# Kernel optimization log

Measured on AMD Instinct MI355X. Metric: run time of the kernel, lower is better.

## Reference

```python
import jax, jax.numpy as jnp
import numpy as np

TAU = 2.0  # aggregator_temp


def setup_inputs() -> dict:
    key = jax.random.key(0)
    k1, k2 = jax.random.split(key)
    B, Na, Nv, D = 32, 512, 256, 384
    audio_feats = jax.random.normal(k1, (B, Na, D), dtype=jnp.float32)
    visual_feats = jax.random.normal(k2, (B, Nv, D), dtype=jnp.float32)
    return {"audio_feats": audio_feats, "visual_feats": visual_feats}


def reference(audio_feats, visual_feats):
    # Cross-batch token similarities: (B, B, Na, Nv)
    # token_sims[i, j, n, m] = <audio_feats[i, n], visual_feats[j, m]>
    token_sims = jnp.einsum('ind,jmd->ijnm', audio_feats, visual_feats)
    # logsumexp_pool: tau * logsumexp(sims / tau) over key-token dim (Nv),
    # then mean over query-token dim (Na) -> clip_sims (B, B)
    aggregator = TAU * jax.nn.logsumexp(token_sims / TAU, axis=-1)
    clip_sims = aggregator.mean(axis=-1)
    return clip_sims
```

## Files before the change

kernel.cpp:

```cpp
#include <hip/hip_runtime.h>

constexpr int B_  = 32;
constexpr int Na  = 512;
constexpr int Nv  = 256;
constexpr int D   = 384;

constexpr int NK2 = D / 64;

constexpr int AGROUPS = B_ * 16;
constexpr int BGROUPS = B_ * 8;
constexpr size_t GROUP_BYTES = 12 * 1024;
constexpr int SCALE_ONE = 0x7F7F7F7F;

typedef int   int4v    __attribute__((ext_vector_type(4)));
typedef int   int8v    __attribute__((ext_vector_type(8)));
typedef float floatx16 __attribute__((ext_vector_type(16)));

__global__ void convert_fp8_kernel(const float* __restrict__ a, const float* __restrict__ v,
                                   unsigned char* __restrict__ a8,
                                   unsigned char* __restrict__ b8,
                                   float* __restrict__ out) {
    int gid = blockIdx.x * blockDim.x + threadIdx.x;
    if (gid < B_ * B_) out[gid] = 0.0f;

    const float* src;
    unsigned char* dst;
    int blk = blockIdx.x;
    if (blk < AGROUPS) {
        src = a + (size_t)blk * 32 * D;
        dst = a8 + (size_t)blk * GROUP_BYTES;
    } else {
        int b2 = blk - AGROUPS;
        src = v + (size_t)b2 * 32 * D;
        dst = b8 + (size_t)b2 * GROUP_BYTES;
    }
    const int t = threadIdx.x;
    const int r = t >> 3, q = t & 7;

    #pragma unroll
    for (int p = 0; p < 3; ++p) {
        int k0 = p * 128 + q * 16;
        const float4* s4 = (const float4*)(src + (size_t)r * D + k0);
        float4 f0 = s4[0], f1 = s4[1], f2 = s4[2], f3 = s4[3];
        int w0 = 0, w1 = 0, w2 = 0, w3 = 0;
        w0 = __builtin_amdgcn_cvt_pk_fp8_f32(f0.x, f0.y, w0, false);
        w0 = __builtin_amdgcn_cvt_pk_fp8_f32(f0.z, f0.w, w0, true);
        w1 = __builtin_amdgcn_cvt_pk_fp8_f32(f1.x, f1.y, w1, false);
        w1 = __builtin_amdgcn_cvt_pk_fp8_f32(f1.z, f1.w, w1, true);
        w2 = __builtin_amdgcn_cvt_pk_fp8_f32(f2.x, f2.y, w2, false);
        w2 = __builtin_amdgcn_cvt_pk_fp8_f32(f2.z, f2.w, w2, true);
        w3 = __builtin_amdgcn_cvt_pk_fp8_f32(f3.x, f3.y, w3, false);
        w3 = __builtin_amdgcn_cvt_pk_fp8_f32(f3.z, f3.w, w3, true);
        int kc = k0 >> 5;
        int h2 = (k0 >> 4) & 1;
        int4v o = { w0, w1, w2, w3 };
        *(int4v*)(dst + (size_t)kc * 1024 + h2 * 512 + r * 16) = o;
    }
}

__device__ __forceinline__ float expsum16(floatx16 a) {
    constexpr float INV_TAU_LN2 = 0.7213475204444817f;
    float e[16];
    #pragma unroll
    for (int i = 0; i < 16; ++i)
        e[i] = __builtin_amdgcn_exp2f(a[i] * INV_TAU_LN2);
    float t0 = (e[0] + e[1])  + (e[2] + e[3]);
    float t1 = (e[4] + e[5])  + (e[6] + e[7]);
    float t2 = (e[8] + e[9])  + (e[10] + e[11]);
    float t3 = (e[12] + e[13]) + (e[14] + e[15]);
    return (t0 + t1) + (t2 + t3);
}

__device__ __forceinline__ int8v mk8(int4v lo, int4v hi) {
    int8v r;
    r[0] = lo[0]; r[1] = lo[1]; r[2] = lo[2]; r[3] = lo[3];
    r[4] = hi[0]; r[5] = hi[1]; r[6] = hi[2]; r[7] = hi[3];
    return r;
}

__global__ __launch_bounds__(256, 3) void gemm_lse_kernel(
        const unsigned char* __restrict__ a8,
        const unsigned char* __restrict__ b8,
        float* __restrict__ out)
{
    __shared__ float ms[4][2][32];

    const int tid  = threadIdx.x;
    const int lane = tid & 63;
    const int vq   = tid >> 6;

    int b = blockIdx.x;
    const int xcd   = b & 7;      b >>= 3;
    const int bi_lo = b & 3;      b >>= 2;
    const int ro    = b & 7;      b >>= 3;
    const int bj    = b;
    const int bi    = xcd * 4 + bi_lo;

    const size_t laneoff = (size_t)lane * 16;
    const unsigned char* pa0 = a8 + (size_t)(bi * 16 + ro * 2) * GROUP_BYTES + laneoff;
    const unsigned char* pa1 = pa0 + GROUP_BYTES;
    const unsigned char* pv0 = b8 + (size_t)(bj * 8 + vq * 2) * GROUP_BYTES + laneoff;
    const unsigned char* pv1 = pv0 + GROUP_BYTES;

    int8v Ab[2][2], Vb[2][2];
    Ab[0][0] = mk8(*(const int4v*)pa0, *(const int4v*)(pa0 + 1024));
    Ab[0][1] = mk8(*(const int4v*)pa1, *(const int4v*)(pa1 + 1024));
    Vb[0][0] = mk8(*(const int4v*)pv0, *(const int4v*)(pv0 + 1024));
    Vb[0][1] = mk8(*(const int4v*)pv1, *(const int4v*)(pv1 + 1024));

    floatx16 acc[2][2];
    #pragma unroll
    for (int ag = 0; ag < 2; ++ag)
        #pragma unroll
        for (int vg = 0; vg < 2; ++vg)
            acc[ag][vg] = (floatx16)(0.0f);

    #pragma unroll
    for (int k = 0; k < NK2; ++k) {
        const int cur = k & 1, nxt = cur ^ 1;
        if (k + 1 < NK2) {
            const size_t o = (size_t)(k + 1) * 2048;
            Ab[nxt][0] = mk8(*(const int4v*)(pa0 + o), *(const int4v*)(pa0 + o + 1024));
            Ab[nxt][1] = mk8(*(const int4v*)(pa1 + o), *(const int4v*)(pa1 + o + 1024));
            Vb[nxt][0] = mk8(*(const int4v*)(pv0 + o), *(const int4v*)(pv0 + o + 1024));
            Vb[nxt][1] = mk8(*(const int4v*)(pv1 + o), *(const int4v*)(pv1 + o + 1024));
        }
        __builtin_amdgcn_sched_barrier(0);
        __builtin_amdgcn_s_setprio(1);
        #pragma unroll
        for (int vg = 0; vg < 2; ++vg) {
            acc[0][vg] = __builtin_amdgcn_mfma_scale_f32_32x32x64_f8f6f4(
                Vb[cur][vg], Ab[cur][0], acc[0][vg], 0, 0, 0, SCALE_ONE, 0, SCALE_ONE);
            acc[1][vg] = __builtin_amdgcn_mfma_scale_f32_32x32x64_f8f6f4(
                Vb[cur][vg], Ab[cur][1], acc[1][vg], 0, 0, 0, SCALE_ONE, 0, SCALE_ONE);
        }
        __builtin_amdgcn_s_setprio(0);
        __builtin_amdgcn_sched_barrier(0);
    }

    float s0 = expsum16(acc[0][0]) + expsum16(acc[0][1]);
    float s1 = expsum16(acc[1][0]) + expsum16(acc[1][1]);
    s0 += __shfl_xor(s0, 32);
    s1 += __shfl_xor(s1, 32);
    if (lane < 32) {
        ms[vq][0][lane] = s0;
        ms[vq][1][lane] = s1;
    }
    __syncthreads();

    if (tid < 64) {
        const int g = tid >> 5, r = tid & 31;
        float e = (ms[0][g][r] + ms[1][g][r]) + (ms[2][g][r] + ms[3][g][r]);
        constexpr float TAU_LN2 = 1.3862943611198906f;
        float lse = TAU_LN2 * __builtin_amdgcn_logf(e);
        #pragma unroll
        for (int m = 1; m < 64; m <<= 1) lse += __shfl_xor(lse, m);
        if (tid == 0)
            atomicAdd(&out[bi * 32 + bj], lse * (1.0f / Na));
    }
}

extern "C" void kernel_launch(void* const* d_in, const int* in_sizes, int n_in,
                              void* d_out, int out_size, void* d_ws, size_t ws_size,
                              hipStream_t stream) {
    const float* audio  = (const float*)d_in[0];
    const float* visual = (const float*)d_in[1];
    float* out = (float*)d_out;

    unsigned char* a8 = (unsigned char*)d_ws;
    unsigned char* b8 = a8 + (size_t)AGROUPS * GROUP_BYTES;

    convert_fp8_kernel<<<dim3(AGROUPS + BGROUPS), dim3(256), 0, stream>>>(
        audio, visual, a8, b8, out);
    gemm_lse_kernel<<<dim3(8192), dim3(256), 0, stream>>>(a8, b8, out);
}
```

Measured before the change: 131.7 us.

## Stage audio tile in LDS via async loads and enlarge blocks to 512 threads

Doubles the block to 8 waves covering 128 audio rows by 256 visual rows. The audio fp8 tile is loaded once per block into 48KB of LDS with global_load_lds, so more waves share it. The visual fp8 layout is changed so each lane reads a contiguous 32-byte int8v per k-step. The explicit register double-buffering and sched barriers are removed, which lowers global traffic for A but adds LDS pressure, an upfront sync, and possibly less overlap of loads with MFMA.

```diff
diff --git a/kernel.cpp b/kernel.cpp
--- a/kernel.cpp
+++ b/kernel.cpp
@@ -16,6 +16,13 @@
 typedef int   int8v    __attribute__((ext_vector_type(8)));
 typedef float floatx16 __attribute__((ext_vector_type(16)));
 
+__device__ __forceinline__ void async_load16(const void* g, void* l) {
+    __builtin_amdgcn_global_load_lds(
+        (const __attribute__((address_space(1))) unsigned int*)g,
+        (__attribute__((address_space(3))) unsigned int*)l,
+        16, 0, 0);
+}
+
 __global__ void convert_fp8_kernel(const float* __restrict__ a, const float* __restrict__ v,
                                    unsigned char* __restrict__ a8,
                                    unsigned char* __restrict__ b8,
@@ -26,7 +33,8 @@
     const float* src;
     unsigned char* dst;
     int blk = blockIdx.x;
-    if (blk < AGROUPS) {
+    const bool isA = blk < AGROUPS;
+    if (isA) {
         src = a + (size_t)blk * 32 * D;
         dst = a8 + (size_t)blk * GROUP_BYTES;
     } else {
@@ -53,8 +61,15 @@
         w3 = __builtin_amdgcn_cvt_pk_fp8_f32(f3.z, f3.w, w3, true);
         int kc = k0 >> 5;
         int h2 = (k0 >> 4) & 1;
+        size_t off;
+        if (isA) {
+            off = (size_t)kc * 1024 + h2 * 512 + r * 16;
+        } else {
+            int q2 = kc >> 1, u = kc & 1, l = r + 32 * h2;
+            off = (size_t)q2 * 2048 + l * 32 + u * 16;
+        }
         int4v o = { w0, w1, w2, w3 };
-        *(int4v*)(dst + (size_t)kc * 1024 + h2 * 512 + r * 16) = o;
+        *(int4v*)(dst + off) = o;
     }
 }
 
@@ -71,42 +86,41 @@
     return (t0 + t1) + (t2 + t3);
 }
 
-__device__ __forceinline__ int8v mk8(int4v lo, int4v hi) {
-    int8v r;
-    r[0] = lo[0]; r[1] = lo[1]; r[2] = lo[2]; r[3] = lo[3];
-    r[4] = hi[0]; r[5] = hi[1]; r[6] = hi[2]; r[7] = hi[3];
-    return r;
-}
-
-__global__ __launch_bounds__(256, 3) void gemm_lse_kernel(
+__global__ __launch_bounds__(512, 4) void gemm_lse_kernel(
         const unsigned char* __restrict__ a8,
         const unsigned char* __restrict__ b8,
         float* __restrict__ out)
 {
-    __shared__ float ms[4][2][32];
+    __shared__ unsigned char ldsA[48 * 1024];
+    __shared__ float ms[4][4][32];
 
     const int tid  = threadIdx.x;
     const int lane = tid & 63;
-    const int vq   = tid >> 6;
+    const int wv   = tid >> 6;
+    const int wm   = wv >> 2;
+    const int wn   = wv & 3;
 
     int b = blockIdx.x;
     const int xcd   = b & 7;      b >>= 3;
     const int bi_lo = b & 3;      b >>= 2;
-    const int ro    = b & 7;      b >>= 3;
+    const int rb    = b & 3;      b >>= 2;
     const int bj    = b;
     const int bi    = xcd * 4 + bi_lo;
 
-    const size_t laneoff = (size_t)lane * 16;
-    const unsigned char* pa0 = a8 + (size_t)(bi * 16 + ro * 2) * GROUP_BYTES + laneoff;
-    const unsigned char* pa1 = pa0 + GROUP_BYTES;
-    const unsigned char* pv0 = b8 + (size_t)(bj * 8 + vq * 2) * GROUP_BYTES + laneoff;
+    const unsigned char* asrc = a8 + (size_t)(bi * 16 + rb * 4) * GROUP_BYTES
+                                   + (size_t)lane * 16;
+    #pragma unroll
+    for (int i = 0; i < 6; ++i) {
+        const int u = wv * 6 + i;
+        async_load16(asrc + (size_t)u * 1024, ldsA + u * 1024);
+    }
+    __syncthreads();
+
+    const unsigned char* pv0 = b8 + (size_t)(bj * 8 + wn * 2) * GROUP_BYTES
+                                  + (size_t)lane * 32;
     const unsigned char* pv1 = pv0 + GROUP_BYTES;
-
-    int8v Ab[2][2], Vb[2][2];
-    Ab[0][0] = mk8(*(const int4v*)pa0, *(const int4v*)(pa0 + 1024));
-    Ab[0][1] = mk8(*(const int4v*)pa1, *(const int4v*)(pa1 + 1024));
-    Vb[0][0] = mk8(*(const int4v*)pv0, *(const int4v*)(pv0 + 1024));
-    Vb[0][1] = mk8(*(const int4v*)pv1, *(const int4v*)(pv1 + 1024));
+    const unsigned char* la  = ldsA + (size_t)(2 * wm) * GROUP_BYTES
+                                    + (size_t)lane * 16;
 
     floatx16 acc[2][2];
     #pragma unroll
@@ -116,26 +130,25 @@
             acc[ag][vg] = (floatx16)(0.0f);
 
     #pragma unroll
-    for (int k = 0; k < NK2; ++k) {
-        const int cur = k & 1, nxt = cur ^ 1;
-        if (k + 1 < NK2) {
-            const size_t o = (size_t)(k + 1) * 2048;
-            Ab[nxt][0] = mk8(*(const int4v*)(pa0 + o), *(const int4v*)(pa0 + o + 1024));
-            Ab[nxt][1] = mk8(*(const int4v*)(pa1 + o), *(const int4v*)(pa1 + o + 1024));
-            Vb[nxt][0] = mk8(*(const int4v*)(pv0 + o), *(const int4v*)(pv0 + o + 1024));
-            Vb[nxt][1] = mk8(*(const int4v*)(pv1 + o), *(const int4v*)(pv1 + o + 1024));
-        }
-        __builtin_amdgcn_sched_barrier(0);
+    for (int q2 = 0; q2 < NK2; ++q2) {
+        int8v V0 = *(const int8v*)(pv0 + (size_t)q2 * 2048);
+        int8v V1 = *(const int8v*)(pv1 + (size_t)q2 * 2048);
+        int4v a0lo = *(const int4v*)(la + (size_t)q2 * 2048);
+        int4v a0hi = *(const int4v*)(la + (size_t)q2 * 2048 + 1024);
+        int4v a1lo = *(const int4v*)(la + GROUP_BYTES + (size_t)q2 * 2048);
+        int4v a1hi = *(const int4v*)(la + GROUP_BYTES + (size_t)q2 * 2048 + 1024);
+        int8v A0 = __builtin_shufflevector(a0lo, a0hi, 0, 1, 2, 3, 4, 5, 6, 7);
+        int8v A1 = __builtin_shufflevector(a1lo, a1hi, 0, 1, 2, 3, 4, 5, 6, 7);
         __builtin_amdgcn_s_setprio(1);
-        #pragma unroll
-        for (int vg = 0; vg < 2; ++vg) {
-            acc[0][vg] = __builtin_amdgcn_mfma_scale_f32_32x32x64_f8f6f4(
-                Vb[cur][vg], Ab[cur][0], acc[0][vg], 0, 0, 0, SCALE_ONE, 0, SCALE_ONE);
-            acc[1][vg] = __builtin_amdgcn_mfma_scale_f32_32x32x64_f8f6f4(
-                Vb[cur][vg], Ab[cur][1], acc[1][vg], 0, 0, 0, SCALE_ONE, 0, SCALE_ONE);
-        }
+        acc[0][0] = __builtin_amdgcn_mfma_scale_f32_32x32x64_f8f6f4(
+            V0, A0, acc[0][0], 0, 0, 0, SCALE_ONE, 0, SCALE_ONE);
+        acc[0][1] = __builtin_amdgcn_mfma_scale_f32_32x32x64_f8f6f4(
+            V1, A0, acc[0][1], 0, 0, 0, SCALE_ONE, 0, SCALE_ONE);
+        acc[1][0] = __builtin_amdgcn_mfma_scale_f32_32x32x64_f8f6f4(
+            V0, A1, acc[1][0], 0, 0, 0, SCALE_ONE, 0, SCALE_ONE);
+        acc[1][1] = __builtin_amdgcn_mfma_scale_f32_32x32x64_f8f6f4(
+            V1, A1, acc[1][1], 0, 0, 0, SCALE_ONE, 0, SCALE_ONE);
         __builtin_amdgcn_s_setprio(0);
-        __builtin_amdgcn_sched_barrier(0);
     }
 
     float s0 = expsum16(acc[0][0]) + expsum16(acc[0][1]);
@@ -143,19 +156,19 @@
     s0 += __shfl_xor(s0, 32);
     s1 += __shfl_xor(s1, 32);
     if (lane < 32) {
-        ms[vq][0][lane] = s0;
-        ms[vq][1][lane] = s1;
+        ms[wn][2 * wm + 0][lane] = s0;
+        ms[wn][2 * wm + 1][lane] = s1;
     }
     __syncthreads();
 
-    if (tid < 64) {
+    if (tid < 128) {
         const int g = tid >> 5, r = tid & 31;
         float e = (ms[0][g][r] + ms[1][g][r]) + (ms[2][g][r] + ms[3][g][r]);
         constexpr float TAU_LN2 = 1.3862943611198906f;
         float lse = TAU_LN2 * __builtin_amdgcn_logf(e);
         #pragma unroll
         for (int m = 1; m < 64; m <<= 1) lse += __shfl_xor(lse, m);
-        if (tid == 0)
+        if ((tid & 63) == 0)
             atomicAdd(&out[bi * 32 + bj], lse * (1.0f / Na));
     }
 }
@@ -172,5 +185,5 @@
 
     convert_fp8_kernel<<<dim3(AGROUPS + BGROUPS), dim3(256), 0, stream>>>(
         audio, visual, a8, b8, out);
-    gemm_lse_kernel<<<dim3(8192), dim3(256), 0, stream>>>(a8, b8, out);
+    gemm_lse_kernel<<<dim3(4096), dim3(512), 0, stream>>>(a8, b8, out);
 }
```

New measurement: 128.6 us. 2.3% less time.
